# Performance work log

Hardware: AMD Instinct MI355X
Metric: run time of the kernel (lower is better)

The kernel has to match this reference:

```python
import jax, jax.numpy as jnp
import numpy as np

D_MODEL = 256
NUM_HEADS = 8
DEPTH = D_MODEL // NUM_HEADS
NEG_BIG = -1e9


def setup_inputs() -> dict:
    key = jax.random.key(0)
    ks = jax.random.split(key, 8)
    B, S = 4, 2048
    inp = {
        "v": jax.random.normal(ks[0], (B, S, D_MODEL), dtype=jnp.float32),
        "k": jax.random.normal(ks[1], (B, S, D_MODEL), dtype=jnp.float32),
        "q": jax.random.normal(ks[2], (B, S, D_MODEL), dtype=jnp.float32),
        "mask": jnp.ones((B, S), dtype=jnp.float32),
        # kernel_size-1 Conv1D without bias == dense projection (d_in, d_out)
        "Wq": jax.random.normal(ks[3], (D_MODEL, D_MODEL), dtype=jnp.float32) * 0.05,
        "Wk": jax.random.normal(ks[4], (D_MODEL, D_MODEL), dtype=jnp.float32) * 0.05,
        "Wv": jax.random.normal(ks[5], (D_MODEL, D_MODEL), dtype=jnp.float32) * 0.05,
        "Wo": jax.random.normal(ks[6], (D_MODEL, D_MODEL), dtype=jnp.float32) * 0.05,
    }
    return inp


def _split_heads(x):
    # (B, S, d_model) -> (B, H, S, depth)
    B, S, _ = x.shape
    return x.reshape(B, S, NUM_HEADS, DEPTH).transpose(0, 2, 1, 3)


def reference(v, k, q, mask, Wq, Wk, Wv, Wo):
    B, S, _ = q.shape
    qh = _split_heads(q @ Wq)  # (B,H,Sq,depth)
    kh = _split_heads(k @ Wk)  # (B,H,Sk,depth)
    vh = _split_heads(v @ Wv)  # (B,H,Sk,depth)

    scale = 1.0 / jnp.sqrt(jnp.asarray(DEPTH, dtype=jnp.float32))
    logits = jnp.einsum("bhqd,bhkd->bhqk", qh, kh) * scale  # (B,H,Sq,Sk)
    mask_att = mask[:, None, None, :]  # broadcast over heads and query dim
    logits = logits + (1.0 - mask_att) * NEG_BIG
    attn = jax.nn.softmax(logits, axis=-1)  # (B,H,Sq,Sk)

    ctx = jnp.einsum("bhqk,bhkd->bhqd", attn, vh)  # (B,H,Sq,depth)
    concat = ctx.transpose(0, 2, 1, 3).reshape(B, S, D_MODEL)
    out = concat @ Wo
    return (out, attn)
```

## Files before the change

### kernel.cpp

```cpp
#include <hip/hip_runtime.h>

#define BB 4
#define HH 8
#define SS 2048
#define DD 32
#define DMODEL 256
#define NEG_BIG_F (-1000000000.0f)
#define SCALE 0.17677669529663687f

typedef short short8 __attribute__((ext_vector_type(8)));
typedef float float4_ __attribute__((ext_vector_type(4)));

__device__ __forceinline__ unsigned short f2bf(float x) {
  unsigned u = __float_as_uint(x);
  u += 0x7FFFu + ((u >> 16) & 1u);
  return (unsigned short)(u >> 16);
}

__global__ __launch_bounds__(256) void prep_w(
    const float* __restrict__ Wq, const float* __restrict__ Wk,
    const float* __restrict__ Wv, const float* __restrict__ Wo,
    unsigned short* __restrict__ wt) {
  __shared__ float tile[32][33];
  int z = blockIdx.z;
  const float* W = (z == 0) ? Wq : (z == 1) ? Wk : (z == 2) ? Wv : Wo;
  unsigned short* dst = wt + (size_t)z * DMODEL * DMODEL;
  int k0 = blockIdx.x * 32, n0 = blockIdx.y * 32;
  int tx = threadIdx.x & 31, ty = threadIdx.x >> 5;
  for (int r = ty; r < 32; r += 8)
    tile[r][tx] = W[(size_t)(k0 + r) * DMODEL + n0 + tx];
  __syncthreads();
  for (int r = ty; r < 32; r += 8)
    dst[(size_t)(n0 + r) * DMODEL + k0 + tx] = f2bf(tile[tx][r]);
}

__global__ __launch_bounds__(256) void proj_kernel(
    const float* __restrict__ q, const float* __restrict__ k,
    const float* __restrict__ v, const unsigned short* __restrict__ wt,
    unsigned short* __restrict__ qh, unsigned short* __restrict__ kh,
    unsigned short* __restrict__ vh) {
  int z = blockIdx.z;
  const float* src = (z == 0) ? q : (z == 1) ? k : v;
  const unsigned short* Wt = wt + (size_t)z * DMODEL * DMODEL;
  unsigned short* dst = (z == 0) ? qh : (z == 1) ? kh : vh;

  int w = threadIdx.x >> 6, lane = threadIdx.x & 63, l16 = lane & 15,
      g = lane >> 4;
  int row = blockIdx.x * 64 + w * 16 + l16;
  int n0 = blockIdx.y * 64;

  float4_ z4 = {0.f, 0.f, 0.f, 0.f};
  float4_ acc[4] = {z4, z4, z4, z4};

  for (int k0 = 0; k0 < DMODEL; k0 += 32) {
    const float4_* ap = (const float4_*)(src + (size_t)row * DMODEL + k0 + 8 * g);
    float4_ a0 = ap[0], a1 = ap[1];
    short8 a;
#pragma unroll
    for (int j = 0; j < 4; ++j) {
      a[j] = (short)f2bf(a0[j]);
      a[4 + j] = (short)f2bf(a1[j]);
    }
#pragma unroll
    for (int cb = 0; cb < 4; ++cb) {
      int n = n0 + cb * 16 + l16;
      short8 bfr = *(const short8*)(Wt + (size_t)n * DMODEL + k0 + 8 * g);
      acc[cb] = __builtin_amdgcn_mfma_f32_16x16x32_bf16(a, bfr, acc[cb], 0, 0, 0);
    }
  }

  int rowbase = blockIdx.x * 64 + w * 16 + 4 * g;
#pragma unroll
  for (int cb = 0; cb < 4; ++cb) {
#pragma unroll
    for (int rr = 0; rr < 4; ++rr) {
      int r = rowbase + rr;
      int c = n0 + cb * 16 + l16;
      int b = r >> 11, s = r & (SS - 1);
      int h = c >> 5, d = c & 31;
      dst[(((size_t)(b * HH + h) * SS + s) * DD) + d] = f2bf(acc[cb][rr]);
    }
  }
}

__global__ __launch_bounds__(256) void fused_attn(
    const unsigned short* __restrict__ qh, const unsigned short* __restrict__ kh,
    const unsigned short* __restrict__ vh, const float* __restrict__ mask,
    float* __restrict__ attn_out, unsigned short* __restrict__ concat) {
  __shared__ float bias[SS];
  __shared__ unsigned short vt[32][72];
  __shared__ unsigned short at[4][16][72];

  int bh = blockIdx.y;
  int b = bh >> 3, h = bh & 7;
  for (int i = threadIdx.x; i < SS; i += 256)
    bias[i] = (1.0f - mask[(size_t)b * SS + i]) * NEG_BIG_F;
  __syncthreads();

  int w = threadIdx.x >> 6, lane = threadIdx.x & 63, l16 = lane & 15,
      g = lane >> 4;
  int q0 = blockIdx.x * 64 + w * 16;

  short8 qa = *(const short8*)(qh + ((size_t)bh * SS + q0 + l16) * DD + 8 * g);

  const unsigned short* kbase = kh + (size_t)bh * SS * DD;
  const unsigned short* vbase = vh + (size_t)bh * SS * DD;
  float4_ z4 = {0.f, 0.f, 0.f, 0.f};

  float m[4], l[4];
#pragma unroll
  for (int i = 0; i < 4; ++i) {
    m[i] = -INFINITY;
    l[i] = 0.f;
  }
#pragma unroll 2
  for (int k0 = 0; k0 < SS; k0 += 16) {
    short8 kf = *(const short8*)(kbase + (size_t)(k0 + l16) * DD + 8 * g);
    float4_ r = __builtin_amdgcn_mfma_f32_16x16x32_bf16(qa, kf, z4, 0, 0, 0);
    float bk = bias[k0 + l16];
#pragma unroll
    for (int rr = 0; rr < 4; ++rr) {
      float t = fmaf(r[rr], SCALE, bk);
      if (t > m[rr]) {
        l[rr] = l[rr] * __expf(m[rr] - t) + 1.0f;
        m[rr] = t;
      } else {
        l[rr] += __expf(t - m[rr]);
      }
    }
  }
#pragma unroll
  for (int off = 1; off < 16; off <<= 1) {
#pragma unroll
    for (int rr = 0; rr < 4; ++rr) {
      float om = __shfl_xor(m[rr], off);
      float ol = __shfl_xor(l[rr], off);
      if (om > m[rr]) {
        l[rr] = l[rr] * __expf(m[rr] - om) + ol;
        m[rr] = om;
      } else {
        l[rr] += ol * __expf(om - m[rr]);
      }
    }
  }
  float rl[4];
#pragma unroll
  for (int rr = 0; rr < 4; ++rr) rl[rr] = 1.0f / l[rr];

  float* arow = attn_out + (size_t)bh * SS * SS;
  float4_ acc0 = z4, acc1 = z4;

  int vr = threadIdx.x >> 2;
  int dseg = (threadIdx.x & 3) * 8;

  for (int kb = 0; kb < SS; kb += 64) {
    __syncthreads();
    {
      short8 vv = *(const short8*)(vbase + (size_t)(kb + vr) * DD + dseg);
#pragma unroll
      for (int j = 0; j < 8; ++j) vt[dseg + j][vr] = (unsigned short)vv[j];
    }
    __syncthreads();

#pragma unroll
    for (int ks = 0; ks < 2; ++ks) {
#pragma unroll
      for (int kt = 0; kt < 2; ++kt) {
        int k0 = kb + ks * 32 + kt * 16;
        short8 kf = *(const short8*)(kbase + (size_t)(k0 + l16) * DD + 8 * g);
        float4_ r = __builtin_amdgcn_mfma_f32_16x16x32_bf16(qa, kf, z4, 0, 0, 0);
        float bk = bias[k0 + l16];
#pragma unroll
        for (int rr = 0; rr < 4; ++rr) {
          float t = fmaf(r[rr], SCALE, bk);
          float p = __expf(t - m[rr]) * rl[rr];
          __builtin_nontemporal_store(
              p, &arow[(size_t)(q0 + 4 * g + rr) * SS + k0 + l16]);
          at[w][4 * g + rr][ks * 32 + kt * 16 + l16] = f2bf(p);
        }
      }
      short8 pa = *(const short8*)&at[w][l16][ks * 32 + 8 * g];
      short8 b0 = *(const short8*)&vt[l16][ks * 32 + 8 * g];
      short8 b1 = *(const short8*)&vt[16 + l16][ks * 32 + 8 * g];
      acc0 = __builtin_amdgcn_mfma_f32_16x16x32_bf16(pa, b0, acc0, 0, 0, 0);
      acc1 = __builtin_amdgcn_mfma_f32_16x16x32_bf16(pa, b1, acc1, 0, 0, 0);
    }
  }

#pragma unroll
  for (int rr = 0; rr < 4; ++rr) {
    int s = q0 + 4 * g + rr;
    size_t base = ((size_t)b * SS + s) * DMODEL + h * DD;
    concat[base + l16] = f2bf(acc0[rr]);
    concat[base + 16 + l16] = f2bf(acc1[rr]);
  }
}

__global__ __launch_bounds__(256) void outgemm_kernel(
    const unsigned short* __restrict__ concat,
    const unsigned short* __restrict__ wot,
    float* __restrict__ out) {
  int w = threadIdx.x >> 6, lane = threadIdx.x & 63, l16 = lane & 15,
      g = lane >> 4;
  int row = blockIdx.x * 64 + w * 16 + l16;
  int n0 = blockIdx.y * 64;
  float4_ z4 = {0.f, 0.f, 0.f, 0.f};
  float4_ acc[4] = {z4, z4, z4, z4};
  for (int k0 = 0; k0 < DMODEL; k0 += 32) {
    short8 a = *(const short8*)(concat + (size_t)row * DMODEL + k0 + 8 * g);
#pragma unroll
    for (int cb = 0; cb < 4; ++cb) {
      int n = n0 + cb * 16 + l16;
      short8 bfr = *(const short8*)(wot + (size_t)n * DMODEL + k0 + 8 * g);
      acc[cb] = __builtin_amdgcn_mfma_f32_16x16x32_bf16(a, bfr, acc[cb], 0, 0, 0);
    }
  }
  int rowbase = blockIdx.x * 64 + w * 16 + 4 * g;
#pragma unroll
  for (int cb = 0; cb < 4; ++cb)
#pragma unroll
    for (int rr = 0; rr < 4; ++rr)
      out[(size_t)(rowbase + rr) * DMODEL + n0 + cb * 16 + l16] = acc[cb][rr];
}

extern "C" void kernel_launch(void* const* d_in, const int* in_sizes, int n_in,
                              void* d_out, int out_size, void* d_ws,
                              size_t ws_size, hipStream_t stream) {
  const float* v = (const float*)d_in[0];
  const float* k = (const float*)d_in[1];
  const float* q = (const float*)d_in[2];
  const float* mask = (const float*)d_in[3];
  const float* Wq = (const float*)d_in[4];
  const float* Wk = (const float*)d_in[5];
  const float* Wv = (const float*)d_in[6];
  const float* Wo = (const float*)d_in[7];

  float* out = (float*)d_out;
  float* attn = out + (size_t)BB * SS * DMODEL;

  const size_t NH = (size_t)BB * HH * SS * DD;
  unsigned short* qh = (unsigned short*)d_ws;
  unsigned short* kh = qh + NH;
  unsigned short* vh = kh + NH;
  unsigned short* concat = vh + NH;
  unsigned short* wt = concat + (size_t)BB * SS * DMODEL;

  prep_w<<<dim3(8, 8, 4), 256, 0, stream>>>(Wq, Wk, Wv, Wo, wt);
  proj_kernel<<<dim3(128, 4, 3), 256, 0, stream>>>(q, k, v, wt, qh, kh, vh);
  fused_attn<<<dim3(32, 32), 256, 0, stream>>>(qh, kh, vh, mask, attn, concat);
  outgemm_kernel<<<dim3(128, 4), 256, 0, stream>>>(
      concat, wt + (size_t)3 * DMODEL * DMODEL, out);
}
```

Before: 277.8 us.

## Transpose score MFMA, use exp2 softmax with folded log-sum-exp, vectorize attn stores

The QK^T MFMA operand order is swapped so each lane holds four consecutive keys for one query row. That lets the attention probabilities be written as float4 vectors and packed bf16 pairs into shared memory. The softmax now works in base 2: scale and bias are prescaled by log2(e), and the online max/sum uses a branchless per-4 update with a wider cross-lane reduction. Normalization is folded into a single log-sum-exp subtraction, which removes the per-element multiply and reciprocal. The nontemporal store hint is dropped in favour of plain vector stores, which may change cache behaviour on the large attn write.

```diff
diff --git a/kernel.cpp b/kernel.cpp
--- a/kernel.cpp
+++ b/kernel.cpp
@@ -7,6 +7,8 @@
 #define DMODEL 256
 #define NEG_BIG_F (-1000000000.0f)
 #define SCALE 0.17677669529663687f
+#define L2E 1.4426950408889634f
+#define SC2 (SCALE * L2E)
 
 typedef short short8 __attribute__((ext_vector_type(8)));
 typedef float float4_ __attribute__((ext_vector_type(4)));
@@ -87,14 +89,14 @@
     const unsigned short* __restrict__ qh, const unsigned short* __restrict__ kh,
     const unsigned short* __restrict__ vh, const float* __restrict__ mask,
     float* __restrict__ attn_out, unsigned short* __restrict__ concat) {
-  __shared__ float bias[SS];
+  __shared__ float biasl2[SS];
   __shared__ unsigned short vt[32][72];
   __shared__ unsigned short at[4][16][72];
 
   int bh = blockIdx.y;
   int b = bh >> 3, h = bh & 7;
   for (int i = threadIdx.x; i < SS; i += 256)
-    bias[i] = (1.0f - mask[(size_t)b * SS + i]) * NEG_BIG_F;
+    biasl2[i] = (1.0f - mask[(size_t)b * SS + i]) * (NEG_BIG_F * L2E);
   __syncthreads();
 
   int w = threadIdx.x >> 6, lane = threadIdx.x & 63, l16 = lane & 15,
@@ -107,47 +109,38 @@
   const unsigned short* vbase = vh + (size_t)bh * SS * DD;
   float4_ z4 = {0.f, 0.f, 0.f, 0.f};
 
-  float m[4], l[4];
-#pragma unroll
-  for (int i = 0; i < 4; ++i) {
-    m[i] = -INFINITY;
-    l[i] = 0.f;
-  }
-#pragma unroll 2
-  for (int k0 = 0; k0 < SS; k0 += 16) {
-    short8 kf = *(const short8*)(kbase + (size_t)(k0 + l16) * DD + 8 * g);
-    float4_ r = __builtin_amdgcn_mfma_f32_16x16x32_bf16(qa, kf, z4, 0, 0, 0);
-    float bk = bias[k0 + l16];
-#pragma unroll
-    for (int rr = 0; rr < 4; ++rr) {
-      float t = fmaf(r[rr], SCALE, bk);
-      if (t > m[rr]) {
-        l[rr] = l[rr] * __expf(m[rr] - t) + 1.0f;
-        m[rr] = t;
-      } else {
-        l[rr] += __expf(t - m[rr]);
-      }
-    }
-  }
-#pragma unroll
-  for (int off = 1; off < 16; off <<= 1) {
-#pragma unroll
-    for (int rr = 0; rr < 4; ++rr) {
-      float om = __shfl_xor(m[rr], off);
-      float ol = __shfl_xor(l[rr], off);
-      if (om > m[rr]) {
-        l[rr] = l[rr] * __expf(m[rr] - om) + ol;
-        m[rr] = om;
-      } else {
-        l[rr] += ol * __expf(om - m[rr]);
-      }
-    }
-  }
-  float rl[4];
-#pragma unroll
-  for (int rr = 0; rr < 4; ++rr) rl[rr] = 1.0f / l[rr];
-
-  float* arow = attn_out + (size_t)bh * SS * SS;
+  float m2 = -INFINITY, l = 0.f;
+  for (int k0 = 0; k0 < SS; k0 += 32) {
+#pragma unroll
+    for (int kk = 0; kk < 2; ++kk) {
+      int kt = k0 + kk * 16;
+      short8 kf = *(const short8*)(kbase + (size_t)(kt + l16) * DD + 8 * g);
+      float4_ r = __builtin_amdgcn_mfma_f32_16x16x32_bf16(kf, qa, z4, 0, 0, 0);
+      float4_ b4 = *(const float4_*)&biasl2[kt + 4 * g];
+      float t0 = fmaf(r[0], SC2, b4[0]);
+      float t1 = fmaf(r[1], SC2, b4[1]);
+      float t2 = fmaf(r[2], SC2, b4[2]);
+      float t3 = fmaf(r[3], SC2, b4[3]);
+      float nm = fmaxf(fmaxf(t0, t1), fmaxf(t2, t3));
+      nm = fmaxf(nm, m2);
+      float s = exp2f(m2 - nm);
+      float e = exp2f(t0 - nm) + exp2f(t1 - nm) + exp2f(t2 - nm) +
+                exp2f(t3 - nm);
+      l = fmaf(l, s, e);
+      m2 = nm;
+    }
+  }
+#pragma unroll
+  for (int off = 16; off < 64; off <<= 1) {
+    float om = __shfl_xor(m2, off);
+    float ol = __shfl_xor(l, off);
+    float nm = fmaxf(m2, om);
+    l = l * exp2f(m2 - nm) + ol * exp2f(om - nm);
+    m2 = nm;
+  }
+  float dq = m2 + log2f(l);
+
+  float* arow = attn_out + (size_t)bh * SS * SS + (size_t)(q0 + l16) * SS;
   float4_ acc0 = z4, acc1 = z4;
 
   int vr = threadIdx.x >> 2;
@@ -166,18 +159,21 @@
     for (int ks = 0; ks < 2; ++ks) {
 #pragma unroll
       for (int kt = 0; kt < 2; ++kt) {
-        int k0 = kb + ks * 32 + kt * 16;
-        short8 kf = *(const short8*)(kbase + (size_t)(k0 + l16) * DD + 8 * g);
-        float4_ r = __builtin_amdgcn_mfma_f32_16x16x32_bf16(qa, kf, z4, 0, 0, 0);
-        float bk = bias[k0 + l16];
-#pragma unroll
-        for (int rr = 0; rr < 4; ++rr) {
-          float t = fmaf(r[rr], SCALE, bk);
-          float p = __expf(t - m[rr]) * rl[rr];
-          __builtin_nontemporal_store(
-              p, &arow[(size_t)(q0 + 4 * g + rr) * SS + k0 + l16]);
-          at[w][4 * g + rr][ks * 32 + kt * 16 + l16] = f2bf(p);
-        }
+        int kk0 = kb + ks * 32 + kt * 16;
+        short8 kf = *(const short8*)(kbase + (size_t)(kk0 + l16) * DD + 8 * g);
+        float4_ r = __builtin_amdgcn_mfma_f32_16x16x32_bf16(kf, qa, z4, 0, 0, 0);
+        float4_ b4 = *(const float4_*)&biasl2[kk0 + 4 * g];
+        float4_ p;
+#pragma unroll
+        for (int rr = 0; rr < 4; ++rr)
+          p[rr] = exp2f(fmaf(r[rr], SC2, b4[rr] - dq));
+        *(float4_*)(arow + kk0 + 4 * g) = p;
+        unsigned u0 = ((unsigned)f2bf(p[1]) << 16) | f2bf(p[0]);
+        unsigned u1 = ((unsigned)f2bf(p[3]) << 16) | f2bf(p[2]);
+        uint2 pk;
+        pk.x = u0;
+        pk.y = u1;
+        *(uint2*)&at[w][l16][ks * 32 + kt * 16 + 4 * g] = pk;
       }
       short8 pa = *(const short8*)&at[w][l16][ks * 32 + 8 * g];
       short8 b0 = *(const short8*)&vt[l16][ks * 32 + 8 * g];
```

Measured after the change: 262.7 us. 5.4% less time.
